# Kernel tuning notes

Measured on AMD Instinct MI355X. Metric: run time of the kernel, lower is better.

## Reference

```python
import jax, jax.numpy as jnp
import numpy as np

LN_EPS = 1e-5


def setup_inputs() -> dict:
    key = jax.random.key(0)
    ks = jax.random.split(key, 5)
    B, I, H = 16384, 512, 512
    x = jax.random.normal(ks[0], (B, I), dtype=jnp.float32)
    h_prev = jax.random.normal(ks[1], (B, H), dtype=jnp.float32)
    c_prev = jax.random.normal(ks[2], (B, H), dtype=jnp.float32)
    # torch nn.Linear weight layout: [out_features, in_features]
    W = jax.random.normal(ks[3], (4 * H, I + H), dtype=jnp.float32) * (1.0 / np.sqrt(I + H))
    b = jnp.zeros((4 * H,), dtype=jnp.float32)
    gamma = jnp.ones((H,), dtype=jnp.float32)
    beta = jnp.zeros((H,), dtype=jnp.float32)
    Wp = jax.random.normal(ks[4], (H, H), dtype=jnp.float32) * (1.0 / np.sqrt(H))
    return {"x": x, "h_prev": h_prev, "c_prev": c_prev, "W": W, "b": b,
            "gamma": gamma, "beta": beta, "Wp": Wp}


def _layernorm(c, gamma, beta):
    mu = jnp.mean(c, axis=-1, keepdims=True)
    var = jnp.mean(jnp.square(c - mu), axis=-1, keepdims=True)
    return (c - mu) * jax.lax.rsqrt(var + LN_EPS) * gamma + beta


def reference(x, h_prev, c_prev, W, b, gamma, beta, Wp):
    # combined: [B, I+H]; gates: [B, 4H]
    combined = jnp.concatenate([x, h_prev], axis=1)
    gates = combined @ W.T + b
    i, f, g, o = jnp.split(gates, 4, axis=1)
    i = jax.nn.sigmoid(i)
    f = jax.nn.sigmoid(f)
    g = jnp.tanh(g)
    o = jax.nn.sigmoid(o)
    cell = f * c_prev + i * g
    cell = _layernorm(cell, gamma, beta)
    out = (o * jnp.tanh(cell)) @ Wp.T  # projection, no bias
    return (out, cell)
```

## Files before the change

### kernel.cpp

```cpp
#include <hip/hip_runtime.h>
#include <hip/hip_bf16.h>


typedef __attribute__((ext_vector_type(4))) float f32x4;
typedef __attribute__((ext_vector_type(8))) short bf16x8;
typedef __attribute__((ext_vector_type(4))) short bf16x4;

#define NB 16384
#define NH 512

__device__ __forceinline__ short f2bf(float f) {
    union { float f; unsigned u; } v; v.f = f;
    unsigned r = v.u + 0x7FFFu + ((v.u >> 16) & 1u);
    return (short)(r >> 16);
}
__device__ __forceinline__ float bf2f(short s) {
    union { unsigned u; float f; } v; v.u = ((unsigned)(unsigned short)s) << 16;
    return v.f;
}
__device__ __forceinline__ float sigmoidf_(float x) {
    return 1.0f / (1.0f + __expf(-x));
}
__device__ __forceinline__ float tanhf_(float x) {
    return 1.0f - 2.0f / (__expf(2.0f * x) + 1.0f);
}

__global__ __launch_bounds__(256, 2)
void k_gates_cell(const float* __restrict__ x, const float* __restrict__ h,
                  const float* __restrict__ c_prev, const float* __restrict__ W,
                  const float* __restrict__ bvec,
                  float* __restrict__ cell_raw, short* __restrict__ o_ws)
{
    __shared__ __align__(16) char lds[128 * 132 * 4];
    short* As = (short*)lds;
    short* Bs = (short*)(lds + 16384);
    float* GT = (float*)lds;

    const int tid  = threadIdx.x;
    const int lane = tid & 63;
    const int wid  = tid >> 6;
    const int wr = wid >> 1, wc = wid & 1;
    const int row0 = blockIdx.x * 128;
    const int h0   = blockIdx.y * 32;

    const f32x4 zero = {0.f, 0.f, 0.f, 0.f};
    f32x4 acc[4][4];
#pragma unroll
    for (int m = 0; m < 4; ++m)
#pragma unroll
        for (int n = 0; n < 4; ++n) acc[m][n] = zero;

    const int scol = (tid & 15) * 4;
    const int srow = tid >> 4;

    for (int kt = 0; kt < 16; ++kt) {
        const int kbase = kt * 64;
        const float* Aptr = (kbase < 512) ? x : h;
        const int kloc = (kbase < 512) ? kbase : (kbase - 512);
        f32x4 av[8], bv[8];
#pragma unroll
        for (int it = 0; it < 8; ++it) {
            const int r = srow + it * 16;
            av[it] = *(const f32x4*)(Aptr + (size_t)(row0 + r) * 512 + kloc + scol);
            const int wrow = ((r >> 5) * 512) + h0 + (r & 31);
            bv[it] = *(const f32x4*)(W + (size_t)wrow * 1024 + kbase + scol);
        }
        __syncthreads();
#pragma unroll
        for (int it = 0; it < 8; ++it) {
            const int r = srow + it * 16;
            bf16x4 pa, pb;
#pragma unroll
            for (int j = 0; j < 4; ++j) { pa[j] = f2bf(av[it][j]); pb[j] = f2bf(bv[it][j]); }
            int byt = r * 128 + scol * 2;
            byt ^= (r & 7) << 4;
            *(bf16x4*)((char*)As + byt) = pa;
            *(bf16x4*)((char*)Bs + byt) = pb;
        }
        __syncthreads();
#pragma unroll
        for (int kk = 0; kk < 64; kk += 32) {
            bf16x8 af[4], bfr[4];
#pragma unroll
            for (int m = 0; m < 4; ++m) {
                const int row = wr * 64 + m * 16 + (lane & 15);
                int byt = row * 128 + (kk + (lane >> 4) * 8) * 2;
                byt ^= (row & 7) << 4;
                af[m] = *(const bf16x8*)((const char*)As + byt);
            }
#pragma unroll
            for (int n = 0; n < 4; ++n) {
                const int row = wc * 64 + n * 16 + (lane & 15);
                int byt = row * 128 + (kk + (lane >> 4) * 8) * 2;
                byt ^= (row & 7) << 4;
                bfr[n] = *(const bf16x8*)((const char*)Bs + byt);
            }
#pragma unroll
            for (int m = 0; m < 4; ++m)
#pragma unroll
                for (int n = 0; n < 4; ++n)
                    acc[m][n] = __builtin_amdgcn_mfma_f32_16x16x32_bf16(af[m], bfr[n], acc[m][n], 0, 0, 0);
        }
    }

    __syncthreads();
#pragma unroll
    for (int m = 0; m < 4; ++m) {
        const int rbase = wr * 64 + m * 16 + ((lane >> 4) * 4);
#pragma unroll
        for (int n = 0; n < 4; ++n) {
            const int col = wc * 64 + n * 16 + (lane & 15);
#pragma unroll
            for (int q = 0; q < 4; ++q)
                GT[(rbase + q) * 132 + col] = acc[m][n][q];
        }
    }
    __syncthreads();

    const int hl = tid & 31;
    const int rb = tid >> 5;
    const float bi  = bvec[        h0 + hl];
    const float bff = bvec[ 512  + h0 + hl];
    const float bg  = bvec[1024  + h0 + hl];
    const float bo  = bvec[1536  + h0 + hl];
#pragma unroll
    for (int it = 0; it < 16; ++it) {
        const int r = rb + it * 8;
        const float iv = GT[r * 132 +       hl] + bi;
        const float fv = GT[r * 132 +  32 + hl] + bff;
        const float gv = GT[r * 132 +  64 + hl] + bg;
        const float ov = GT[r * 132 +  96 + hl] + bo;
        const size_t idx = (size_t)(row0 + r) * 512 + h0 + hl;
        const float c = c_prev[idx];
        cell_raw[idx] = sigmoidf_(fv) * c + sigmoidf_(iv) * tanhf_(gv);
        o_ws[idx] = f2bf(sigmoidf_(ov));
    }
}

__global__ __launch_bounds__(64)
void k_layernorm(const float* __restrict__ gamma, const float* __restrict__ beta,
                 float* __restrict__ cell, const short* __restrict__ o_ws,
                 short* __restrict__ s_ws)
{
    const int r = blockIdx.x;
    const int lane = threadIdx.x;
    float* row = cell + (size_t)r * 512;
    f32x4 v0 = *(const f32x4*)(row + lane * 8);
    f32x4 v1 = *(const f32x4*)(row + lane * 8 + 4);
    float s1 = 0.f, s2 = 0.f;
#pragma unroll
    for (int j = 0; j < 4; ++j) {
        s1 += v0[j] + v1[j];
        s2 += v0[j] * v0[j] + v1[j] * v1[j];
    }
#pragma unroll
    for (int off = 32; off > 0; off >>= 1) {
        s1 += __shfl_xor(s1, off);
        s2 += __shfl_xor(s2, off);
    }
    const float mu  = s1 * (1.f / 512.f);
    const float var = s2 * (1.f / 512.f) - mu * mu;
    const float rs  = rsqrtf(var + 1e-5f);
    const f32x4 g0 = *(const f32x4*)(gamma + lane * 8);
    const f32x4 g1 = *(const f32x4*)(gamma + lane * 8 + 4);
    const f32x4 b0 = *(const f32x4*)(beta + lane * 8);
    const f32x4 b1 = *(const f32x4*)(beta + lane * 8 + 4);
    const bf16x8 o8 = *(const bf16x8*)(o_ws + (size_t)r * 512 + lane * 8);
    f32x4 c0, c1; bf16x8 s8;
#pragma unroll
    for (int j = 0; j < 4; ++j) {
        c0[j] = (v0[j] - mu) * rs * g0[j] + b0[j];
        c1[j] = (v1[j] - mu) * rs * g1[j] + b1[j];
    }
#pragma unroll
    for (int j = 0; j < 4; ++j) {
        s8[j]     = f2bf(bf2f(o8[j])     * tanhf_(c0[j]));
        s8[j + 4] = f2bf(bf2f(o8[j + 4]) * tanhf_(c1[j]));
    }
    *(f32x4*)(row + lane * 8)     = c0;
    *(f32x4*)(row + lane * 8 + 4) = c1;
    *(bf16x8*)(s_ws + (size_t)r * 512 + lane * 8) = s8;
}

__global__ __launch_bounds__(256, 2)
void k_proj(const short* __restrict__ s_ws, const float* __restrict__ Wp,
            float* __restrict__ out)
{
    __shared__ __align__(16) short As[128 * 64];
    __shared__ __align__(16) short Bs[128 * 64];
    const int tid = threadIdx.x;
    const int lane = tid & 63;
    const int wid = tid >> 6;
    const int wr = wid >> 1, wc = wid & 1;
    const int row0 = blockIdx.x * 128;
    const int col0 = blockIdx.y * 128;

    const f32x4 zero = {0.f, 0.f, 0.f, 0.f};
    f32x4 acc[4][4];
#pragma unroll
    for (int m = 0; m < 4; ++m)
#pragma unroll
        for (int n = 0; n < 4; ++n) acc[m][n] = zero;

    const int acol = (tid & 7) * 8;
    const int arow = tid >> 3;
    const int scol = (tid & 15) * 4;
    const int srow = tid >> 4;

    for (int kt = 0; kt < 8; ++kt) {
        const int kbase = kt * 64;
        bf16x8 sa[4]; f32x4 bv[8];
#pragma unroll
        for (int it = 0; it < 4; ++it) {
            const int r = arow + it * 32;
            sa[it] = *(const bf16x8*)(s_ws + (size_t)(row0 + r) * 512 + kbase + acol);
        }
#pragma unroll
        for (int it = 0; it < 8; ++it) {
            const int r = srow + it * 16;
            bv[it] = *(const f32x4*)(Wp + (size_t)(col0 + r) * 512 + kbase + scol);
        }
        __syncthreads();
#pragma unroll
        for (int it = 0; it < 4; ++it) {
            const int r = arow + it * 32;
            int byt = r * 128 + acol * 2;
            byt ^= (r & 7) << 4;
            *(bf16x8*)((char*)As + byt) = sa[it];
        }
#pragma unroll
        for (int it = 0; it < 8; ++it) {
            const int r = srow + it * 16;
            bf16x4 pb;
#pragma unroll
            for (int j = 0; j < 4; ++j) pb[j] = f2bf(bv[it][j]);
            int byt = r * 128 + scol * 2;
            byt ^= (r & 7) << 4;
            *(bf16x4*)((char*)Bs + byt) = pb;
        }
        __syncthreads();
#pragma unroll
        for (int kk = 0; kk < 64; kk += 32) {
            bf16x8 af[4], bfr[4];
#pragma unroll
            for (int m = 0; m < 4; ++m) {
                const int row = wr * 64 + m * 16 + (lane & 15);
                int byt = row * 128 + (kk + (lane >> 4) * 8) * 2;
                byt ^= (row & 7) << 4;
                af[m] = *(const bf16x8*)((const char*)As + byt);
            }
#pragma unroll
            for (int n = 0; n < 4; ++n) {
                const int row = wc * 64 + n * 16 + (lane & 15);
                int byt = row * 128 + (kk + (lane >> 4) * 8) * 2;
                byt ^= (row & 7) << 4;
                bfr[n] = *(const bf16x8*)((const char*)Bs + byt);
            }
#pragma unroll
            for (int m = 0; m < 4; ++m)
#pragma unroll
                for (int n = 0; n < 4; ++n)
                    acc[m][n] = __builtin_amdgcn_mfma_f32_16x16x32_bf16(af[m], bfr[n], acc[m][n], 0, 0, 0);
        }
    }

#pragma unroll
    for (int m = 0; m < 4; ++m) {
        const int grow = row0 + wr * 64 + m * 16 + ((lane >> 4) * 4);
#pragma unroll
        for (int n = 0; n < 4; ++n) {
            const int gcol = col0 + wc * 64 + n * 16 + (lane & 15);
#pragma unroll
            for (int q = 0; q < 4; ++q)
                out[(size_t)(grow + q) * 512 + gcol] = acc[m][n][q];
        }
    }
}

extern "C" void kernel_launch(void* const* d_in, const int* in_sizes, int n_in,
                              void* d_out, int out_size, void* d_ws, size_t ws_size,
                              hipStream_t stream) {
    (void)in_sizes; (void)n_in; (void)out_size; (void)ws_size;
    const float* x      = (const float*)d_in[0];
    const float* h_prev = (const float*)d_in[1];
    const float* c_prev = (const float*)d_in[2];
    const float* W      = (const float*)d_in[3];
    const float* bvec   = (const float*)d_in[4];
    const float* gamma  = (const float*)d_in[5];
    const float* beta   = (const float*)d_in[6];
    const float* Wp     = (const float*)d_in[7];

    float* out  = (float*)d_out;
    float* cell = out + (size_t)NB * NH;
    short* o_ws = (short*)d_ws;
    short* s_ws = o_ws + (size_t)NB * NH;

    dim3 g1(NB / 128, NH / 32);
    k_gates_cell<<<g1, 256, 0, stream>>>(x, h_prev, c_prev, W, bvec, cell, o_ws);
    k_layernorm<<<NB, 64, 0, stream>>>(gamma, beta, cell, o_ws, s_ws);
    dim3 g3(NB / 128, NH / 128);
    k_proj<<<g3, 256, 0, stream>>>(s_ws, Wp, out);
}
```

Before: 315.3 us.

## Pre-convert operands to bf16 and stream GEMM tiles directly into LDS

```diff
diff --git a/kernel.cpp b/kernel.cpp
--- a/kernel.cpp
+++ b/kernel.cpp
@@ -18,23 +18,61 @@
     union { unsigned u; float f; } v; v.u = ((unsigned)(unsigned short)s) << 16;
     return v.f;
 }
-__device__ __forceinline__ float sigmoidf_(float x) {
-    return 1.0f / (1.0f + __expf(-x));
-}
-__device__ __forceinline__ float tanhf_(float x) {
-    return 1.0f - 2.0f / (__expf(2.0f * x) + 1.0f);
-}
-
-__global__ __launch_bounds__(256, 2)
-void k_gates_cell(const float* __restrict__ x, const float* __restrict__ h,
-                  const float* __restrict__ c_prev, const float* __restrict__ W,
-                  const float* __restrict__ bvec,
+__device__ __forceinline__ float sigmoidf_(float x) { return 1.0f / (1.0f + __expf(-x)); }
+__device__ __forceinline__ float tanhf_(float x) { return 1.0f - 2.0f / (__expf(2.0f * x) + 1.0f); }
+
+__device__ __forceinline__ void gld16(const void* g, void* l) {
+    __builtin_amdgcn_global_load_lds(
+        (const __attribute__((address_space(1))) void*)g,
+        (__attribute__((address_space(3))) void*)l, 16, 0, 0);
+}
+
+__global__ __launch_bounds__(256)
+void k_convert_A(const float* __restrict__ x, const float* __restrict__ h,
+                 short* __restrict__ Abf)
+{
+    const long long total = (long long)NB * 256;
+    long long i = (long long)blockIdx.x * 256 + threadIdx.x;
+    const long long stride = (long long)gridDim.x * 256;
+    for (; i < total; i += stride) {
+        const int r  = (int)(i >> 8);
+        const int c4 = (int)(i & 255);
+        const float* src = (c4 < 128) ? (x + (size_t)r * 512 + c4 * 4)
+                                      : (h + (size_t)r * 512 + (c4 - 128) * 4);
+        f32x4 v = *(const f32x4*)src;
+        bf16x4 o;
+#pragma unroll
+        for (int j = 0; j < 4; ++j) o[j] = f2bf(v[j]);
+        *(bf16x4*)(Abf + i * 4) = o;
+    }
+}
+
+__global__ __launch_bounds__(256)
+void k_convert_W(const float* __restrict__ W, const float* __restrict__ Wp,
+                 short* __restrict__ Wbf, short* __restrict__ Wpbf)
+{
+    const long long nW  = (long long)2048 * 1024 / 4;
+    const long long nWp = (long long)512 * 512 / 4;
+    long long i = (long long)blockIdx.x * 256 + threadIdx.x;
+    const long long stride = (long long)gridDim.x * 256;
+    for (; i < nW + nWp; i += stride) {
+        f32x4 v; short* dst;
+        if (i < nW) { v = *(const f32x4*)(W + i * 4); dst = Wbf + i * 4; }
+        else { v = *(const f32x4*)(Wp + (i - nW) * 4); dst = Wpbf + (i - nW) * 4; }
+        bf16x4 o;
+#pragma unroll
+        for (int j = 0; j < 4; ++j) o[j] = f2bf(v[j]);
+        *(bf16x4*)dst = o;
+    }
+}
+
+__global__ __launch_bounds__(256, 3)
+void k_gates_cell(const short* __restrict__ Abf, const short* __restrict__ Wbf,
+                  const float* __restrict__ c_prev, const float* __restrict__ bvec,
                   float* __restrict__ cell_raw, short* __restrict__ o_ws)
 {
-    __shared__ __align__(16) char lds[128 * 132 * 4];
-    short* As = (short*)lds;
-    short* Bs = (short*)(lds + 16384);
-    float* GT = (float*)lds;
+    __shared__ __align__(16) short As[128 * 64];
+    __shared__ __align__(16) short Bs[128 * 64];
 
     const int tid  = threadIdx.x;
     const int lane = tid & 63;
@@ -50,32 +88,23 @@
 #pragma unroll
         for (int n = 0; n < 4; ++n) acc[m][n] = zero;
 
-    const int scol = (tid & 15) * 4;
-    const int srow = tid >> 4;
+    const int k8 = ((lane & 7) ^ (lane >> 3)) * 8;
+    int aOff[4], bOff[4];
+#pragma unroll
+    for (int j = 0; j < 4; ++j) {
+        const int row = (wid * 4 + j) * 8 + (lane >> 3);
+        aOff[j] = (row0 + row) * 1024 + k8;
+        const int gate = (row >> 4) & 3;
+        const int wrow = gate * 512 + h0 + (row >> 6) * 16 + (row & 15);
+        bOff[j] = wrow * 1024 + k8;
+    }
 
     for (int kt = 0; kt < 16; ++kt) {
         const int kbase = kt * 64;
-        const float* Aptr = (kbase < 512) ? x : h;
-        const int kloc = (kbase < 512) ? kbase : (kbase - 512);
-        f32x4 av[8], bv[8];
-#pragma unroll
-        for (int it = 0; it < 8; ++it) {
-            const int r = srow + it * 16;
-            av[it] = *(const f32x4*)(Aptr + (size_t)(row0 + r) * 512 + kloc + scol);
-            const int wrow = ((r >> 5) * 512) + h0 + (r & 31);
-            bv[it] = *(const f32x4*)(W + (size_t)wrow * 1024 + kbase + scol);
-        }
-        __syncthreads();
-#pragma unroll
-        for (int it = 0; it < 8; ++it) {
-            const int r = srow + it * 16;
-            bf16x4 pa, pb;
-#pragma unroll
-            for (int j = 0; j < 4; ++j) { pa[j] = f2bf(av[it][j]); pb[j] = f2bf(bv[it][j]); }
-            int byt = r * 128 + scol * 2;
-            byt ^= (r & 7) << 4;
-            *(bf16x4*)((char*)As + byt) = pa;
-            *(bf16x4*)((char*)Bs + byt) = pb;
+#pragma unroll
+        for (int j = 0; j < 4; ++j) {
+            gld16(Abf + aOff[j] + kbase, As + (wid * 4 + j) * 512);
+            gld16(Wbf + bOff[j] + kbase, Bs + (wid * 4 + j) * 512);
         }
         __syncthreads();
 #pragma unroll
@@ -101,49 +130,36 @@
                 for (int n = 0; n < 4; ++n)
                     acc[m][n] = __builtin_amdgcn_mfma_f32_16x16x32_bf16(af[m], bfr[n], acc[m][n], 0, 0, 0);
         }
-    }
-
-    __syncthreads();
+        __syncthreads();
+    }
+
+    const int hcol = h0 + wc * 16 + (lane & 15);
+    float bias[4];
+#pragma unroll
+    for (int n = 0; n < 4; ++n) bias[n] = bvec[n * 512 + hcol];
 #pragma unroll
     for (int m = 0; m < 4; ++m) {
-        const int rbase = wr * 64 + m * 16 + ((lane >> 4) * 4);
-#pragma unroll
-        for (int n = 0; n < 4; ++n) {
-            const int col = wc * 64 + n * 16 + (lane & 15);
-#pragma unroll
-            for (int q = 0; q < 4; ++q)
-                GT[(rbase + q) * 132 + col] = acc[m][n][q];
-        }
-    }
-    __syncthreads();
-
-    const int hl = tid & 31;
-    const int rb = tid >> 5;
-    const float bi  = bvec[        h0 + hl];
-    const float bff = bvec[ 512  + h0 + hl];
-    const float bg  = bvec[1024  + h0 + hl];
-    const float bo  = bvec[1536  + h0 + hl];
-#pragma unroll
-    for (int it = 0; it < 16; ++it) {
-        const int r = rb + it * 8;
-        const float iv = GT[r * 132 +       hl] + bi;
-        const float fv = GT[r * 132 +  32 + hl] + bff;
-        const float gv = GT[r * 132 +  64 + hl] + bg;
-        const float ov = GT[r * 132 +  96 + hl] + bo;
-        const size_t idx = (size_t)(row0 + r) * 512 + h0 + hl;
-        const float c = c_prev[idx];
-        cell_raw[idx] = sigmoidf_(fv) * c + sigmoidf_(iv) * tanhf_(gv);
-        o_ws[idx] = f2bf(sigmoidf_(ov));
-    }
-}
-
-__global__ __launch_bounds__(64)
+        const int rbase = row0 + wr * 64 + m * 16 + ((lane >> 4) * 4);
+#pragma unroll
+        for (int q = 0; q < 4; ++q) {
+            const size_t idx = (size_t)(rbase + q) * 512 + hcol;
+            const float iv = acc[m][0][q] + bias[0];
+            const float fv = acc[m][1][q] + bias[1];
+            const float gv = acc[m][2][q] + bias[2];
+            const float ov = acc[m][3][q] + bias[3];
+            const float c = c_prev[idx];
+            cell_raw[idx] = sigmoidf_(fv) * c + sigmoidf_(iv) * tanhf_(gv);
+            o_ws[idx] = f2bf(sigmoidf_(ov));
+        }
+    }
+}
+
+__global__ __launch_bounds__(256)
 void k_layernorm(const float* __restrict__ gamma, const float* __restrict__ beta,
-                 float* __restrict__ cell, const short* __restrict__ o_ws,
-                 short* __restrict__ s_ws)
-{
-    const int r = blockIdx.x;
-    const int lane = threadIdx.x;
+                 float* __restrict__ cell, short* __restrict__ s_io)
+{
+    const int r = blockIdx.x * 4 + (threadIdx.x >> 6);
+    const int lane = threadIdx.x & 63;
     float* row = cell + (size_t)r * 512;
     f32x4 v0 = *(const f32x4*)(row + lane * 8);
     f32x4 v1 = *(const f32x4*)(row + lane * 8 + 4);
@@ -165,7 +181,7 @@
     const f32x4 g1 = *(const f32x4*)(gamma + lane * 8 + 4);
     const f32x4 b0 = *(const f32x4*)(beta + lane * 8);
     const f32x4 b1 = *(const f32x4*)(beta + lane * 8 + 4);
-    const bf16x8 o8 = *(const bf16x8*)(o_ws + (size_t)r * 512 + lane * 8);
+    const bf16x8 o8 = *(const bf16x8*)(s_io + (size_t)r * 512 + lane * 8);
     f32x4 c0, c1; bf16x8 s8;
 #pragma unroll
     for (int j = 0; j < 4; ++j) {
@@ -179,11 +195,11 @@
     }
     *(f32x4*)(row + lane * 8)     = c0;
     *(f32x4*)(row + lane * 8 + 4) = c1;
-    *(bf16x8*)(s_ws + (size_t)r * 512 + lane * 8) = s8;
-}
-
-__global__ __launch_bounds__(256, 2)
-void k_proj(const short* __restrict__ s_ws, const float* __restrict__ Wp,
+    *(bf16x8*)(s_io + (size_t)r * 512 + lane * 8) = s8;
+}
+
+__global__ __launch_bounds__(256, 3)
+void k_proj(const short* __restrict__ s_ws, const short* __restrict__ Wpbf,
             float* __restrict__ out)
 {
     __shared__ __align__(16) short As[128 * 64];
@@ -202,41 +218,21 @@
 #pragma unroll
         for (int n = 0; n < 4; ++n) acc[m][n] = zero;
 
-    const int acol = (tid & 7) * 8;
-    const int arow = tid >> 3;
-    const int scol = (tid & 15) * 4;
-    const int srow = tid >> 4;
+    const int k8 = ((lane & 7) ^ (lane >> 3)) * 8;
+    int aOff[4], bOff[4];
+#pragma unroll
+    for (int j = 0; j < 4; ++j) {
+        const int row = (wid * 4 + j) * 8 + (lane >> 3);
+        aOff[j] = (row0 + row) * 512 + k8;
+        bOff[j] = (col0 + row) * 512 + k8;
+    }
 
     for (int kt = 0; kt < 8; ++kt) {
         const int kbase = kt * 64;
-        bf16x8 sa[4]; f32x4 bv[8];
-#pragma unroll
-        for (int it = 0; it < 4; ++it) {
-            const int r = arow + it * 32;
-            sa[it] = *(const bf16x8*)(s_ws + (size_t)(row0 + r) * 512 + kbase + acol);
-        }
-#pragma unroll
-        for (int it = 0; it < 8; ++it) {
-            const int r = srow + it * 16;
-            bv[it] = *(const f32x4*)(Wp + (size_t)(col0 + r) * 512 + kbase + scol);
-        }
-        __syncthreads();
-#pragma unroll
-        for (int it = 0; it < 4; ++it) {
-            const int r = arow + it * 32;
-            int byt = r * 128 + acol * 2;
-            byt ^= (r & 7) << 4;
-            *(bf16x8*)((char*)As + byt) = sa[it];
-        }
-#pragma unroll
-        for (int it = 0; it < 8; ++it) {
-            const int r = srow + it * 16;
-            bf16x4 pb;
-#pragma unroll
-            for (int j = 0; j < 4; ++j) pb[j] = f2bf(bv[it][j]);
-            int byt = r * 128 + scol * 2;
-            byt ^= (r & 7) << 4;
-            *(bf16x4*)((char*)Bs + byt) = pb;
+#pragma unroll
+        for (int j = 0; j < 4; ++j) {
+            gld16(s_ws + aOff[j] + kbase, As + (wid * 4 + j) * 512);
+            gld16(Wpbf + bOff[j] + kbase, Bs + (wid * 4 + j) * 512);
         }
         __syncthreads();
 #pragma unroll
@@ -262,6 +258,7 @@
                 for (int n = 0; n < 4; ++n)
                     acc[m][n] = __builtin_amdgcn_mfma_f32_16x16x32_bf16(af[m], bfr[n], acc[m][n], 0, 0, 0);
         }
+        __syncthreads();
     }
 
 #pragma unroll
@@ -292,12 +289,16 @@
 
     float* out  = (float*)d_out;
     float* cell = out + (size_t)NB * NH;
-    short* o_ws = (short*)d_ws;
-    short* s_ws = o_ws + (size_t)NB * NH;
-
-    dim3 g1(NB / 128, NH / 32);
-    k_gates_cell<<<g1, 256, 0, stream>>>(x, h_prev, c_prev, W, bvec, cell, o_ws);
-    k_layernorm<<<NB, 64, 0, stream>>>(gamma, beta, cell, o_ws, s_ws);
+    short* Abf  = (short*)d_out;
+    short* s_io = (short*)d_ws;
+    short* Wbf  = s_io + (size_t)NB * NH;
+    short* Wpbf = Wbf + (size_t)2048 * 1024;
+
+    k_convert_A<<<2048, 256, 0, stream>>>(x, h_prev, Abf);
+    k_convert_W<<<1024, 256, 0, stream>>>(W, Wp, Wbf, Wpbf);
+    dim3 g1(NB / 128, 2048 / 128);
+    k_gates_cell<<<g1, 256, 0, stream>>>(Abf, Wbf, c_prev, bvec, cell, s_io);
+    k_layernorm<<<NB / 4, 256, 0, stream>>>(gamma, beta, cell, s_io);
     dim3 g3(NB / 128, NH / 128);
-    k_proj<<<g3, 256, 0, stream>>>(s_ws, Wp, out);
-}
+    k_proj<<<g3, 256, 0, stream>>>(s_io, Wpbf, out);
+}
```

After: 264.6 us. -16.1%, faster.
